# Kernel optimization log

Measured on AMD Instinct MI355X. Metric: run time of the kernel, lower is better.

The kernel has to match this reference:

```python
import jax, jax.numpy as jnp
import numpy as np

N_NODES = 10000
N_EDGES = 640000
D = 128
BN_EPS = 1e-5


def setup_inputs() -> dict:
    key = jax.random.key(0)
    k1, k2, k3 = jax.random.split(key, 3)
    x = jax.random.normal(k1, (N_NODES, D), dtype=jnp.float32)
    edge_index = jax.random.randint(k2, (2, N_EDGES), 0, N_NODES, dtype=jnp.int64)
    W = jax.random.normal(k3, (D, D), dtype=jnp.float32) * (1.0 / np.sqrt(D))
    b = jnp.zeros((D,), dtype=jnp.float32)
    gamma = jnp.ones((D,), dtype=jnp.float32)
    beta = jnp.zeros((D,), dtype=jnp.float32)
    return {"x": x, "edge_index": edge_index, "W": W, "b": b, "gamma": gamma, "beta": beta}


def reference(x, edge_index, W, b, gamma, beta):
    # GINConv: out_i = MLP((1+eps)*x_i + sum_{j->i} x_j), eps=0
    src = edge_index[0]
    dst = edge_index[1]
    agg = jax.ops.segment_sum(x[src], dst, num_segments=N_NODES)  # [N, D]
    h = agg + x  # (1 + eps) * x with eps = 0
    # MLP inside GINConv: Linear + ReLU
    h = jnp.maximum(h @ W + b, 0.0)
    # outer F.relu (idempotent after inner ReLU, kept for faithfulness)
    h = jnp.maximum(h, 0.0)
    # BatchNorm1d, training-mode batch statistics (biased variance)
    mean = jnp.mean(h, axis=0)
    var = jnp.var(h, axis=0)
    h = (h - mean) * jax.lax.rsqrt(var + BN_EPS) * gamma + beta
    # Dropout in eval mode -> identity. his_x = [h]; return the main output.
    return h
```

## Files before the change

kernel.cpp:

```cpp
#include <hip/hip_runtime.h>

#define N_NODES 10000
#define N_EDGES 640000
#define D 128
#define BN_EPS 1e-5f
#define CAP 128
#define NSTRIPE 16
#define RPB 8
#define NB 1250
#define NBC 157
#define BCAPC 4608
#define ABLK 256
#define ASLICE 2500
#define CSENT 1250

typedef _Float16 half8_t __attribute__((ext_vector_type(8)));
typedef float f32x4 __attribute__((ext_vector_type(4)));
typedef unsigned short u16;

static __device__ __forceinline__ float rdlane(float v, int k) {
    return __uint_as_float(__builtin_amdgcn_readlane(__float_as_uint(v), k));
}

__global__ __launch_bounds__(256) void k_bin(
    const int* __restrict__ ei,
    const float4* __restrict__ x4,
    int* cur,
    int* __restrict__ recs,
    half8_t* __restrict__ xh)
{
    __shared__ int cnt[NBC];
    __shared__ int base_[NBC];
    __shared__ int loff[NBC];
    __shared__ int sc[256];
    __shared__ int sorted[ASLICE];
    const int b = blockIdx.x, t = threadIdx.x;

    {
        const int n8 = N_NODES * D / 8;
        for (int i = b * 256 + t; i < n8; i += ABLK * 256) {
            const float4 a = x4[2 * i];
            const float4 c = x4[2 * i + 1];
            half8_t h;
            h[0] = (_Float16)a.x; h[1] = (_Float16)a.y;
            h[2] = (_Float16)a.z; h[3] = (_Float16)a.w;
            h[4] = (_Float16)c.x; h[5] = (_Float16)c.y;
            h[6] = (_Float16)c.z; h[7] = (_Float16)c.w;
            xh[i] = h;
        }
    }
    if (b == 0 && t < 16) {
        half8_t z;
        #pragma unroll
        for (int i = 0; i < 8; i++) z[i] = (_Float16)0.0f;
        xh[N_NODES * 16 + t] = z;
    }

    if (t < NBC) cnt[t] = 0;
    __syncthreads();

    const int e0 = b * ASLICE;
    for (int i = t; i < ASLICE; i += 256)
        atomicAdd(&cnt[ei[N_EDGES + e0 + i] >> 6], 1);
    __syncthreads();

    sc[t] = (t < NBC) ? cnt[t] : 0;
    __syncthreads();
    #pragma unroll
    for (int off = 1; off < 256; off <<= 1) {
        const int add = (t >= off) ? sc[t - off] : 0;
        __syncthreads();
        sc[t] += add;
        __syncthreads();
    }

    const unsigned cbase = (unsigned)cur[CSENT];
    if (t < NBC) {
        loff[t]  = sc[t] - cnt[t];
        base_[t] = (int)((unsigned)atomicAdd(&cur[t], cnt[t]) - cbase);
        cnt[t]   = 0;
    }
    __syncthreads();

    for (int i = t; i < ASLICE; i += 256) {
        const int e = e0 + i;
        const int d = ei[N_EDGES + e];
        const int s = ei[e];
        const int bin = d >> 6;
        const int p = atomicAdd(&cnt[bin], 1);
        sorted[loff[bin] + p] = (s << 6) | (d & 63);
    }
    __syncthreads();

    const int g = t >> 4, sl = t & 15;
    for (int bin = g; bin < NBC; bin += 16) {
        const int c  = cnt[bin];
        const int gb = base_[bin];
        const int lo = loff[bin];
        for (int k = sl; k < c; k += 16) {
            const int pos = gb + k;
            if (pos < BCAPC) recs[bin * BCAPC + pos] = sorted[lo + k];
        }
    }
}

__global__ __launch_bounds__(256, 4) void k_gfill(
    const float* __restrict__ x,
    const half8_t* __restrict__ xh8,
    const int* __restrict__ cur,
    const int* __restrict__ recs,
    const float* __restrict__ W,
    const float* __restrict__ bias,
    float* __restrict__ out,
    float* __restrict__ stats)
{
    __shared__ u16 lst[RPB * CAP];
    __shared__ int cnt[RPB];
    __shared__ float hs[RPB][D];
    const int tid  = threadIdx.x;
    const int bin  = blockIdx.x;
    const int cb   = bin >> 3;
    const int sub  = bin & 7;
    const int wv   = tid >> 6;
    const int lane = tid & 63;
    const int qq   = lane >> 4;
    const int l    = lane & 15;
    const float4* __restrict__ x4 = (const float4*)x;

    if (tid < RPB) cnt[tid] = 0;
    __syncthreads();

    const unsigned cbase = (unsigned)cur[CSENT];
    int nrec = (int)((unsigned)cur[cb] - cbase);
    if (nrec > BCAPC) nrec = BCAPC;
    const int* __restrict__ br = recs + cb * BCAPC;
    for (int i = tid; i < nrec; i += 256) {
        const int r = br[i];
        if (((r >> 3) & 7) == sub) {
            const int p = atomicAdd(&cnt[r & 7], 1);
            if (p < CAP) lst[(r & 7) * CAP + p] = (u16)(r >> 6);
        }
    }
    __syncthreads();

    {
        const int nd = tid >> 5;
        const int k0 = tid & 31;
        int c = cnt[nd]; if (c > CAP) c = CAP;
        const int pc = (c + 63) & ~63;
        for (int k = c + k0; k < pc; k += 32)
            lst[nd * CAP + k] = (u16)N_NODES;
    }
    __syncthreads();

    #pragma unroll
    for (int j = 0; j < 2; j++) {
        const int lrow = wv * 2 + j;
        const int node = bin * RPB + lrow;
        int n = cnt[lrow];
        if (n > CAP) n = CAP;
        const int np = (n + 63) & ~63;
        const u16* __restrict__ myl = &lst[lrow * CAP];
        float acc[8];
        #pragma unroll
        for (int z = 0; z < 8; z++) acc[z] = 0.f;

        for (int g = 0; g < np; g += 64) {
            half8_t v[16];
            #pragma unroll
            for (int u = 0; u < 16; u++) {
                const int s = (int)myl[g + 4 * u + qq];
                v[u] = xh8[(size_t)s * 16 + l];
            }
            #pragma unroll
            for (int u = 0; u < 16; u++)
                #pragma unroll
                for (int z = 0; z < 8; z++)
                    acc[z] += (float)v[u][z];
        }
        #pragma unroll
        for (int z = 0; z < 8; z++) {
            acc[z] += __shfl_xor(acc[z], 16, 64);
            acc[z] += __shfl_xor(acc[z], 32, 64);
        }
        if (qq == 0) {
            const float4 xa = x4[(size_t)node * 32 + 2 * l];
            const float4 xb = x4[(size_t)node * 32 + 2 * l + 1];
            *(float4*)&hs[lrow][8 * l] =
                make_float4(acc[0] + xa.x, acc[1] + xa.y, acc[2] + xa.z, acc[3] + xa.w);
            *(float4*)&hs[lrow][8 * l + 4] =
                make_float4(acc[4] + xb.x, acc[5] + xb.y, acc[6] + xb.z, acc[7] + xb.w);
        }
    }
    __syncthreads();

    const int col = tid & 127;
    const int rg  = tid >> 7;
    float hlo[4], hhi[4];
    #pragma unroll
    for (int r = 0; r < 4; r++) {
        hlo[r] = hs[rg * 4 + r][lane];
        hhi[r] = hs[rg * 4 + r][64 + lane];
    }
    float a[4] = {0.f, 0.f, 0.f, 0.f};
    const float* __restrict__ wc = W + col;
    #pragma unroll 8
    for (int k = 0; k < 64; k++) {
        const float w = wc[k * D];
        #pragma unroll
        for (int r = 0; r < 4; r++)
            a[r] = fmaf(rdlane(hlo[r], k), w, a[r]);
    }
    #pragma unroll 8
    for (int k = 0; k < 64; k++) {
        const float w = wc[(64 + k) * D];
        #pragma unroll
        for (int r = 0; r < 4; r++)
            a[r] = fmaf(rdlane(hhi[r], k), w, a[r]);
    }

    const float bcol = bias[col];
    float s1 = 0.f, s2 = 0.f;
    #pragma unroll
    for (int r = 0; r < 4; r++) {
        const float v = fmaxf(a[r] + bcol, 0.f);
        __builtin_nontemporal_store(v, &out[(size_t)(bin * RPB + rg * 4 + r) * D + col]);
        s1 += v;
        s2 += v * v;
    }

    __syncthreads();
    float* red = &hs[0][0];
    red[tid]       = s1;
    red[256 + tid] = s2;
    __syncthreads();
    if (tid < D) {
        float* sp = &stats[(size_t)(bin & (NSTRIPE - 1)) * 256];
        atomicAdd(&sp[tid],     red[tid]       + red[tid + 128]);
        atomicAdd(&sp[D + tid], red[256 + tid] + red[256 + tid + 128]);
    }
}

__global__ __launch_bounds__(256) void k_bn(
    float* out,
    const float* __restrict__ stats,
    const float* __restrict__ gamma,
    const float* __restrict__ beta)
{
    __shared__ float sc_[D], sh[D];
    const int tid = threadIdx.x;
    if (tid < D) {
        const float fbase = stats[NSTRIPE * 256];
        float s = 0.f, q = 0.f;
        #pragma unroll
        for (int cp = 0; cp < NSTRIPE; cp++) {
            s += stats[cp * 256 + tid]     - fbase;
            q += stats[cp * 256 + D + tid] - fbase;
        }
        const float mean = s * (1.0f / N_NODES);
        const float var  = q * (1.0f / N_NODES) - mean * mean;
        const float scale = gamma[tid] * rsqrtf(var + BN_EPS);
        sc_[tid] = scale;
        sh[tid] = beta[tid] - mean * scale;
    }
    __syncthreads();

    f32x4* o4 = (f32x4*)out;
    #pragma unroll
    for (int j = 0; j < 2; j++) {
        const int f = blockIdx.x * 512 + j * 256 + tid;
        const int c = (f & 31) << 2;
        f32x4 v = __builtin_nontemporal_load(&o4[f]);
        v.x = v.x * sc_[c]     + sh[c];
        v.y = v.y * sc_[c + 1] + sh[c + 1];
        v.z = v.z * sc_[c + 2] + sh[c + 2];
        v.w = v.w * sc_[c + 3] + sh[c + 3];
        __builtin_nontemporal_store(v, &o4[f]);
    }
}

extern "C" void kernel_launch(void* const* d_in, const int* in_sizes, int n_in,
                              void* d_out, int out_size, void* d_ws, size_t ws_size,
                              hipStream_t stream)
{
    const float* x     = (const float*)d_in[0];
    const int*   ei    = (const int*)d_in[1];
    const float* W     = (const float*)d_in[2];
    const float* bias  = (const float*)d_in[3];
    const float* gamma = (const float*)d_in[4];
    const float* beta  = (const float*)d_in[5];
    float* out = (float*)d_out;

    float*   stats = (float*)d_ws;
    int*     cur   = (int*)(stats + NSTRIPE * 256 + 8);
    int*     recs  = cur + 1280;
    half8_t* xh    = (half8_t*)(recs + NBC * BCAPC);

    k_bin<<<ABLK, 256, 0, stream>>>(ei, (const float4*)x, cur, recs, xh);
    k_gfill<<<NB, 256, 0, stream>>>(x, xh, cur, recs, W, bias, out, stats);
    k_bn<<<N_NODES * D / 2048, 256, 0, stream>>>(out, stats, gamma, beta);
}
```

Measured before the change: 126.9 us.

## Gather two node rows per wave jointly and read hs from LDS in GEMV

The neighbor gather now processes both of a wave's destination rows in one interleaved loop, with padding to a 32 multiple of the larger count instead of 64 per row. This raises memory-level parallelism and cuts padded dummy loads. The small matmul replaces readlane broadcasts from registers with direct LDS broadcast reads of hs. The launch-bounds occupancy hint is dropped. Together these trade register pressure and LDS traffic for fewer wasted gathers and scalar readlane ops.

```diff
diff --git a/kernel.cpp b/kernel.cpp
--- a/kernel.cpp
+++ b/kernel.cpp
@@ -18,10 +18,6 @@
 typedef float f32x4 __attribute__((ext_vector_type(4)));
 typedef unsigned short u16;
 
-static __device__ __forceinline__ float rdlane(float v, int k) {
-    return __uint_as_float(__builtin_amdgcn_readlane(__float_as_uint(v), k));
-}
-
 __global__ __launch_bounds__(256) void k_bin(
     const int* __restrict__ ei,
     const float4* __restrict__ x4,
@@ -104,7 +100,7 @@
     }
 }
 
-__global__ __launch_bounds__(256, 4) void k_gfill(
+__global__ __launch_bounds__(256) void k_gfill(
     const float* __restrict__ x,
     const half8_t* __restrict__ xh8,
     const int* __restrict__ cur,
@@ -146,77 +142,79 @@
     {
         const int nd = tid >> 5;
         const int k0 = tid & 31;
-        int c = cnt[nd]; if (c > CAP) c = CAP;
-        const int pc = (c + 63) & ~63;
-        for (int k = c + k0; k < pc; k += 32)
+        int c  = cnt[nd];     if (c  > CAP) c  = CAP;
+        int cp = cnt[nd ^ 1]; if (cp > CAP) cp = CAP;
+        const int m  = c > cp ? c : cp;
+        const int L  = (m + 31) & ~31;
+        for (int k = c + k0; k < L; k += 32)
             lst[nd * CAP + k] = (u16)N_NODES;
     }
     __syncthreads();
 
-    #pragma unroll
-    for (int j = 0; j < 2; j++) {
-        const int lrow = wv * 2 + j;
-        const int node = bin * RPB + lrow;
-        int n = cnt[lrow];
-        if (n > CAP) n = CAP;
-        const int np = (n + 63) & ~63;
-        const u16* __restrict__ myl = &lst[lrow * CAP];
-        float acc[8];
-        #pragma unroll
-        for (int z = 0; z < 8; z++) acc[z] = 0.f;
-
-        for (int g = 0; g < np; g += 64) {
-            half8_t v[16];
+    {
+        int n0 = cnt[2 * wv];     if (n0 > CAP) n0 = CAP;
+        int n1 = cnt[2 * wv + 1]; if (n1 > CAP) n1 = CAP;
+        const int m = n0 > n1 ? n0 : n1;
+        const int L = (m + 31) & ~31;
+        const u16* __restrict__ l0 = &lst[(2 * wv) * CAP];
+        const u16* __restrict__ l1 = &lst[(2 * wv + 1) * CAP];
+        float acc0[8], acc1[8];
+        #pragma unroll
+        for (int z = 0; z < 8; z++) { acc0[z] = 0.f; acc1[z] = 0.f; }
+
+        for (int g = 0; g < L; g += 32) {
+            half8_t v0[8], v1[8];
             #pragma unroll
-            for (int u = 0; u < 16; u++) {
-                const int s = (int)myl[g + 4 * u + qq];
-                v[u] = xh8[(size_t)s * 16 + l];
+            for (int u = 0; u < 8; u++) {
+                const int s0 = (int)l0[g + 4 * u + qq];
+                const int s1 = (int)l1[g + 4 * u + qq];
+                v0[u] = xh8[(size_t)s0 * 16 + l];
+                v1[u] = xh8[(size_t)s1 * 16 + l];
             }
             #pragma unroll
-            for (int u = 0; u < 16; u++)
+            for (int u = 0; u < 8; u++) {
                 #pragma unroll
-                for (int z = 0; z < 8; z++)
-                    acc[z] += (float)v[u][z];
+                for (int z = 0; z < 8; z++) {
+                    acc0[z] += (float)v0[u][z];
+                    acc1[z] += (float)v1[u][z];
+                }
+            }
         }
         #pragma unroll
         for (int z = 0; z < 8; z++) {
-            acc[z] += __shfl_xor(acc[z], 16, 64);
-            acc[z] += __shfl_xor(acc[z], 32, 64);
+            acc0[z] += __shfl_xor(acc0[z], 16, 64);
+            acc0[z] += __shfl_xor(acc0[z], 32, 64);
+            acc1[z] += __shfl_xor(acc1[z], 16, 64);
+            acc1[z] += __shfl_xor(acc1[z], 32, 64);
         }
         if (qq == 0) {
-            const float4 xa = x4[(size_t)node * 32 + 2 * l];
-            const float4 xb = x4[(size_t)node * 32 + 2 * l + 1];
-            *(float4*)&hs[lrow][8 * l] =
-                make_float4(acc[0] + xa.x, acc[1] + xa.y, acc[2] + xa.z, acc[3] + xa.w);
-            *(float4*)&hs[lrow][8 * l + 4] =
-                make_float4(acc[4] + xb.x, acc[5] + xb.y, acc[6] + xb.z, acc[7] + xb.w);
+            const int node0 = bin * RPB + 2 * wv;
+            const float4 xa = x4[(size_t)node0 * 32 + 2 * l];
+            const float4 xb = x4[(size_t)node0 * 32 + 2 * l + 1];
+            *(float4*)&hs[2 * wv][8 * l] =
+                make_float4(acc0[0] + xa.x, acc0[1] + xa.y, acc0[2] + xa.z, acc0[3] + xa.w);
+            *(float4*)&hs[2 * wv][8 * l + 4] =
+                make_float4(acc0[4] + xb.x, acc0[5] + xb.y, acc0[6] + xb.z, acc0[7] + xb.w);
+            const int node1 = node0 + 1;
+            const float4 xc = x4[(size_t)node1 * 32 + 2 * l];
+            const float4 xd = x4[(size_t)node1 * 32 + 2 * l + 1];
+            *(float4*)&hs[2 * wv + 1][8 * l] =
+                make_float4(acc1[0] + xc.x, acc1[1] + xc.y, acc1[2] + xc.z, acc1[3] + xc.w);
+            *(float4*)&hs[2 * wv + 1][8 * l + 4] =
+                make_float4(acc1[4] + xd.x, acc1[5] + xd.y, acc1[6] + xd.z, acc1[7] + xd.w);
         }
     }
     __syncthreads();
 
     const int col = tid & 127;
     const int rg  = tid >> 7;
-    float hlo[4], hhi[4];
-    #pragma unroll
-    for (int r = 0; r < 4; r++) {
-        hlo[r] = hs[rg * 4 + r][lane];
-        hhi[r] = hs[rg * 4 + r][64 + lane];
-    }
     float a[4] = {0.f, 0.f, 0.f, 0.f};
-    const float* __restrict__ wc = W + col;
     #pragma unroll 8
-    for (int k = 0; k < 64; k++) {
-        const float w = wc[k * D];
+    for (int k = 0; k < D; k++) {
+        const float w = W[k * D + col];
         #pragma unroll
         for (int r = 0; r < 4; r++)
-            a[r] = fmaf(rdlane(hlo[r], k), w, a[r]);
-    }
-    #pragma unroll 8
-    for (int k = 0; k < 64; k++) {
-        const float w = wc[(64 + k) * D];
-        #pragma unroll
-        for (int r = 0; r < 4; r++)
-            a[r] = fmaf(rdlane(hhi[r], k), w, a[r]);
+            a[r] = fmaf(hs[rg * 4 + r][k], w, a[r]);
     }
 
     const float bcol = bias[col];
```

Result: faster. 123.0 us (-3.0%).
